# Kernel optimization log

Hardware: AMD Instinct MI355X
Metric: run time of the kernel (lower is better)

Reference implementation:

```python
import jax, jax.numpy as jnp
import numpy as np

B, S, D, DK, DV = 8, 2048, 256, 128, 128

def setup_inputs() -> dict:
    key = jax.random.key(0)
    ks = jax.random.split(key, 9)
    return {
        "x_q": jax.random.normal(ks[0], (B, S, D), jnp.float32),
        "x_k": jax.random.normal(ks[1], (B, S, D), jnp.float32),
        "x_v": jax.random.normal(ks[2], (B, S, D), jnp.float32),
        "Wq": jax.random.normal(ks[3], (D, DK), jnp.float32) * (1.0 / np.sqrt(D)),
        "bq": jax.random.normal(ks[4], (DK,), jnp.float32) * 0.02,
        "Wk": jax.random.normal(ks[5], (D, DK), jnp.float32) * (1.0 / np.sqrt(D)),
        "bk": jax.random.normal(ks[6], (DK,), jnp.float32) * 0.02,
        "Wv": jax.random.normal(ks[7], (D, DV), jnp.float32) * (1.0 / np.sqrt(D)),
        "bv": jax.random.normal(ks[8], (DV,), jnp.float32) * 0.02,
    }

def reference(x_q, x_k, x_v, Wq, bq, Wk, bk, Wv, bv):
    # Dense projections: [B,S,D] @ [D,dk] + bias
    q = jnp.einsum("bsd,dk->bsk", x_q, Wq) + bq
    k = jnp.einsum("bsd,dk->bsk", x_k, Wk) + bk
    v = jnp.einsum("bsd,dv->bsv", x_v, Wv) + bv
    scale = 1.0 / np.sqrt(Wq.shape[1]).astype(np.float32)  # 1/sqrt(d_k)
    scores = jnp.einsum("bqk,bsk->bqs", q, k) * scale       # [B,S,S]
    attn = jax.nn.softmax(scores, axis=-1)
    return jnp.einsum("bqs,bsv->bqv", attn, v)               # [B,S,d_v]
```

## Files before the change

kernel.cpp:

```cpp
#include <hip/hip_runtime.h>
#include <stdint.h>

typedef float    f32x4 __attribute__((ext_vector_type(4)));
typedef _Float16 f16x8 __attribute__((ext_vector_type(8)));
typedef _Float16 f16x4 __attribute__((ext_vector_type(4)));
typedef unsigned int u32x4 __attribute__((ext_vector_type(4)));

#define SPLIT 4
#define NTILES 8

__device__ __forceinline__ f32x4 mfma16(f16x8 a, f16x8 b, f32x4 c) {
    return __builtin_amdgcn_mfma_f32_16x16x32_f16(a, b, c, 0, 0, 0);
}
__device__ __forceinline__ f32x4 mfma16k16(f16x4 a, f16x4 b, f32x4 c) {
    return __builtin_amdgcn_mfma_f32_16x16x16f16(a, b, c, 0, 0, 0);
}
__device__ __forceinline__ void gll16(const _Float16* g, _Float16* l) {
    __builtin_amdgcn_global_load_lds(
        (const __attribute__((address_space(1))) void*)g,
        (__attribute__((address_space(3))) void*)l, 16, 0, 0);
}

__global__ __launch_bounds__(256) void prep_weights(
    const float* __restrict__ Wq, const float* __restrict__ Wk,
    const float* __restrict__ Wv, _Float16* __restrict__ wt) {
    __shared__ float Ls[64 * 65];
    const int bx = blockIdx.x;
    const int w  = bx >> 3, t = bx & 7;
    const int k0 = (t >> 1) * 64, n0 = (t & 1) * 64;
    const float* W = (w == 0) ? Wq : (w == 1) ? Wk : Wv;
    const int tid = threadIdx.x;
    #pragma unroll
    for (int i = 0; i < 16; i++) {
        int idx = i * 256 + tid;
        int r = idx >> 6, c = idx & 63;
        Ls[r * 65 + c] = W[(k0 + r) * 128 + n0 + c];
    }
    __syncthreads();
    #pragma unroll
    for (int i = 0; i < 16; i++) {
        int idx = i * 256 + tid;
        int r2 = idx >> 6, c2 = idx & 63;
        wt[w * 32768 + (n0 + r2) * 256 + k0 + c2] = (_Float16)Ls[c2 * 65 + r2];
    }
}

__global__ __launch_bounds__(256) void proj_kernel(
    const float* __restrict__ xq, const float* __restrict__ xk,
    const float* __restrict__ xv, const _Float16* __restrict__ wt,
    const float* __restrict__ bq, const float* __restrict__ bk,
    const float* __restrict__ bv,
    _Float16* __restrict__ qo, _Float16* __restrict__ ko,
    _Float16* __restrict__ vtmp)
{
    const int mode = blockIdx.y;
    const float*    X    = mode == 0 ? xq : mode == 1 ? xk : xv;
    const float*    bias = mode == 0 ? bq : mode == 1 ? bk : bv;
    const _Float16* W    = wt + mode * 32768;
    _Float16*       Y    = mode == 0 ? qo : mode == 1 ? ko : vtmp;

    const int tid  = threadIdx.x;
    const int wave = tid >> 6, lane = tid & 63;
    const int ln   = lane & 15, qd = lane >> 4;
    const int row0 = blockIdx.x * 64 + wave * 16;

    const float*    xrow = X + (size_t)(row0 + ln) * 256 + qd * 8;
    const _Float16* wb   = W + ln * 256 + qd * 8;

    f32x4 acc[8];
    #pragma unroll
    for (int i = 0; i < 8; i++) acc[i] = (f32x4){0.f, 0.f, 0.f, 0.f};

    #pragma unroll
    for (int kk = 0; kk < 8; kk++) {
        f32x4 a0 = *(const f32x4*)(xrow + kk * 32);
        f32x4 a1 = *(const f32x4*)(xrow + kk * 32 + 4);
        f16x8 af;
        af[0] = (_Float16)a0[0]; af[1] = (_Float16)a0[1];
        af[2] = (_Float16)a0[2]; af[3] = (_Float16)a0[3];
        af[4] = (_Float16)a1[0]; af[5] = (_Float16)a1[1];
        af[6] = (_Float16)a1[2]; af[7] = (_Float16)a1[3];
        #pragma unroll
        for (int nt = 0; nt < 8; nt++) {
            f16x8 bf = *(const f16x8*)(wb + nt * 4096 + kk * 32);
            acc[nt] = mfma16(af, bf, acc[nt]);
        }
    }

    const float SC = 0.08838834764831845f * 1.4426950408889634f;
    #pragma unroll
    for (int nt = 0; nt < 8; nt++) {
        int col = nt * 16 + ln;
        float bb = bias[col];
        #pragma unroll
        for (int r = 0; r < 4; r++) {
            int orow = row0 + qd * 4 + r;
            float val = acc[nt][r] + bb;
            if (mode == 0) val *= SC;
            Y[(size_t)orow * 128 + col] = (_Float16)val;
        }
    }
}

__global__ __launch_bounds__(256) void transpose_v(
    const _Float16* __restrict__ vtmp, _Float16* __restrict__ vt)
{
    __shared__ __align__(16) _Float16 Ls[64 * 72];
    const int b  = blockIdx.z;
    const int s0 = blockIdx.x * 64;
    const int d0 = blockIdx.y * 64;
    const int tid = threadIdx.x;
    #pragma unroll
    for (int i = 0; i < 2; i++) {
        int idx = i * 256 + tid;
        int r = idx >> 3, c = (idx & 7) * 8;
        *(f16x8*)&Ls[r * 72 + c] =
            *(const f16x8*)(vtmp + (size_t)(b * 2048 + s0 + r) * 128 + d0 + c);
    }
    __syncthreads();
    #pragma unroll
    for (int i = 0; i < 2; i++) {
        int idx = i * 256 + tid;
        int dr = idx >> 3, sc8 = (idx & 7) * 8;
        f16x8 o;
        #pragma unroll
        for (int j = 0; j < 8; j++) o[j] = Ls[(sc8 + j) * 72 + dr];
        *(f16x8*)(vt + (size_t)(b * 128 + d0 + dr) * 2048 + s0 + sc8) = o;
    }
}

__global__ __launch_bounds__(512, 4) void attn_kernel(
    const _Float16* __restrict__ qp, const _Float16* __restrict__ kp,
    const _Float16* __restrict__ vtp, _Float16* __restrict__ opart,
    float2* __restrict__ ml)
{
    const int bid = blockIdx.x;
    const int gx  = bid & 7;
    const int q0i = (bid >> 3) & 15;
    const int gg  = bid >> 7;
    const int g   = gg * 8 + gx;
    const int b   = g >> 2;
    const int z   = g & 3;
    const int q0  = q0i * 128;

    const int tid  = threadIdx.x;
    const int wave = tid >> 6, lane = tid & 63;
    const int ln   = lane & 15, qd = lane >> 4;

    __shared__ __align__(16) _Float16 smem[32768];

    const _Float16* qrow =
        qp + (size_t)(b * 2048 + q0 + wave * 16 + ln) * 128 + qd * 8;
    f16x8 qf[4];
    #pragma unroll
    for (int c = 0; c < 4; c++) qf[c] = *(const f16x8*)(qrow + c * 32);

    f32x4 o[8];
    #pragma unroll
    for (int i = 0; i < 8; i++) o[i] = (f32x4){0.f, 0.f, 0.f, 0.f};
    float m_run = -1e30f, l_run = 0.f;

    const _Float16* kbase = kp + (size_t)b * 2048 * 128;
    const _Float16* vbase = vtp + (size_t)b * 128 * 2048;
    const int kt0 = z * NTILES;

    auto stage = [&](int kt, int buf) {
        const _Float16* ks = kbase + (size_t)kt * 64 * 128;
        const _Float16* vs = vbase + kt * 64;
        _Float16* kdst0 = smem + buf * 8192;
        _Float16* vdst0 = smem + 16384 + buf * 8192;
        #pragma unroll
        for (int j = 0; j < 2; j++) {
            int p  = wave * 128 + j * 64 + lane;
            int r  = p >> 4, cp = p & 15;
            int cl = cp ^ (r & 15);
            gll16(ks + r * 128 + cl * 8, kdst0 + (wave * 128 + j * 64) * 8);
            int dv = p >> 3, cq = p & 7;
            int c2 = cq ^ (dv & 7);
            gll16(vs + (size_t)dv * 2048 + c2 * 8, vdst0 + (wave * 128 + j * 64) * 8);
        }
    };

    stage(kt0, 0);

    for (int it = 0; it < NTILES; it++) {
        __syncthreads();
        if (it + 1 < NTILES) stage(kt0 + it + 1, (it + 1) & 1);
        const _Float16* kb = smem + (it & 1) * 8192;
        const _Float16* vb = smem + 16384 + (it & 1) * 8192;

        f32x4 sc[4];
        #pragma unroll
        for (int st = 0; st < 4; st++) {
            sc[st] = (f32x4){0.f, 0.f, 0.f, 0.f};
            int base = (st * 16 + ln) * 128;
            #pragma unroll
            for (int c = 0; c < 4; c++) {
                f16x8 kf = *(const f16x8*)&kb[base + ((c * 4 + qd) ^ ln) * 8];
                sc[st] = mfma16(kf, qf[c], sc[st]);
            }
        }

        float t = sc[0][0];
        #pragma unroll
        for (int st = 0; st < 4; st++)
            #pragma unroll
            for (int r = 0; r < 4; r++) t = fmaxf(t, sc[st][r]);
        t = fmaxf(t, __shfl_xor(t, 16));
        t = fmaxf(t, __shfl_xor(t, 32));
        const float mnew  = fmaxf(m_run, t);
        const float alpha = exp2f(m_run - mnew);

        f16x4 ph[4];
        float ssum = 0.f;
        #pragma unroll
        for (int st = 0; st < 4; st++) {
            #pragma unroll
            for (int r = 0; r < 4; r++) {
                float p = exp2f(sc[st][r] - mnew);
                ssum += p;
                ph[st][r] = (_Float16)p;
            }
        }
        ssum += __shfl_xor(ssum, 16);
        ssum += __shfl_xor(ssum, 32);
        l_run = l_run * alpha + ssum;
        m_run = mnew;

        #pragma unroll
        for (int dt = 0; dt < 8; dt++)
            #pragma unroll
            for (int r = 0; r < 4; r++) o[dt][r] *= alpha;

        #pragma unroll
        for (int st = 0; st < 4; st++) {
            #pragma unroll
            for (int dt = 0; dt < 8; dt++) {
                f16x4 vf = *(const f16x4*)&vb[(dt * 16 + ln) * 64 +
                           ((st * 2 + (qd >> 1)) ^ (ln & 7)) * 8 + (qd & 1) * 4];
                o[dt] = mfma16k16(vf, ph[st], o[dt]);
            }
        }
    }

    __syncthreads();
    _Float16* pw = smem + wave * 2176;
    #pragma unroll
    for (int dt = 0; dt < 8; dt++) {
        f16x4 h;
        #pragma unroll
        for (int r = 0; r < 4; r++) h[r] = (_Float16)o[dt][r];
        *(f16x4*)&pw[ln * 136 + dt * 16 + qd * 4] = h;
    }
    const size_t prow = (size_t)(z * 8 + b) * 2048 + q0 + wave * 16;
    __builtin_amdgcn_s_waitcnt(0);
    #pragma unroll
    for (int i = 0; i < 4; i++) {
        int row = i * 4 + qd;
        f16x8 vrow = *(const f16x8*)&pw[row * 136 + ln * 8];
        *(f16x8*)(opart + (prow + row) * 128 + ln * 8) = vrow;
    }
    if (qd == 0) {
        float2 v; v.x = m_run; v.y = l_run;
        ml[prow + ln] = v;
    }
}

__global__ __launch_bounds__(256) void merge_kernel(
    const _Float16* __restrict__ opart, const float2* __restrict__ ml,
    float* __restrict__ out)
{
    const int t = threadIdx.x;
    const int r = t >> 4, cg = t & 15;
    const size_t row = (size_t)blockIdx.x * 16 + r;

    float M = -1e30f;
    #pragma unroll
    for (int zi = 0; zi < SPLIT; zi++)
        M = fmaxf(M, ml[(size_t)zi * 16384 + row].x);
    float L = 0.f;
    float acc[8] = {0.f, 0.f, 0.f, 0.f, 0.f, 0.f, 0.f, 0.f};
    #pragma unroll
    for (int zi = 0; zi < SPLIT; zi++) {
        float2 p = ml[(size_t)zi * 16384 + row];
        float w = exp2f(p.x - M);
        L += w * p.y;
        f16x8 v = *(const f16x8*)&opart[((size_t)zi * 16384 + row) * 128 + cg * 8];
        #pragma unroll
        for (int j = 0; j < 8; j++) acc[j] += w * (float)v[j];
    }
    const float inv = 1.0f / L;
    float* op = out + row * 128 + cg * 8;
    f32x4 lo = (f32x4){acc[0] * inv, acc[1] * inv, acc[2] * inv, acc[3] * inv};
    f32x4 hi = (f32x4){acc[4] * inv, acc[5] * inv, acc[6] * inv, acc[7] * inv};
    *(f32x4*)op = lo;
    *(f32x4*)(op + 4) = hi;
}

extern "C" void kernel_launch(void* const* d_in, const int* in_sizes, int n_in,
                              void* d_out, int out_size, void* d_ws, size_t ws_size,
                              hipStream_t stream) {
    const float* xq = (const float*)d_in[0];
    const float* xk = (const float*)d_in[1];
    const float* xv = (const float*)d_in[2];
    const float* Wq = (const float*)d_in[3];
    const float* bq = (const float*)d_in[4];
    const float* Wk = (const float*)d_in[5];
    const float* bk = (const float*)d_in[6];
    const float* Wv = (const float*)d_in[7];
    const float* bv = (const float*)d_in[8];
    float* out = (float*)d_out;

    char* ws = (char*)d_ws;
    _Float16* wt    = (_Float16*)ws;
    _Float16* qo    = (_Float16*)(ws + 196608);
    _Float16* ko    = (_Float16*)(ws + 196608 + 4194304);
    _Float16* vt    = (_Float16*)(ws + 196608 + 2 * 4194304);
    float2*   ml    = (float2*)  (ws + 196608 + 3 * 4194304);
    _Float16* opart = (_Float16*)(ws + 196608 + 3 * 4194304 + 1048576);
    _Float16* vtmp  = opart;

    hipLaunchKernelGGL(prep_weights, dim3(24), dim3(256), 0, stream,
                       Wq, Wk, Wv, wt);
    hipLaunchKernelGGL(proj_kernel, dim3(256, 3), dim3(256), 0, stream,
                       xq, xk, xv, wt, bq, bk, bv, qo, ko, vtmp);
    hipLaunchKernelGGL(transpose_v, dim3(32, 2, 8), dim3(256), 0, stream,
                       vtmp, vt);
    hipLaunchKernelGGL(attn_kernel, dim3(16 * 8 * SPLIT), dim3(512), 0, stream,
                       qo, ko, vt, opart, ml);
    hipLaunchKernelGGL(merge_kernel, dim3(1024), dim3(256), 0, stream,
                       opart, ml, out);
}
```

Measured before the change: 164.0 us.

## Switch attention to 32x32x16 MFMA tiles with 8-way KV split

Rewrites the attention kernel around 32x32x16 f16 MFMAs, so each wave owns 32 query rows and processes 32-key tiles, up from 16x16 MFMAs on 16 rows. P fragments are exchanged between half-waves with a shuffle so they can feed the PV MFMA. The block shrinks to 256 threads with a smaller LDS footprint, and the KV split goes from 4 to 8, doubling the grid. The aim is fewer MFMA and LDS instructions per FLOP and better occupancy. In exchange, the partial-output traffic and merge work double, and the V tile layout in LDS is no longer XOR-swizzled, which may cause bank conflicts.

```diff
diff --git a/kernel.cpp b/kernel.cpp
--- a/kernel.cpp
+++ b/kernel.cpp
@@ -1,19 +1,20 @@
 #include <hip/hip_runtime.h>
 #include <stdint.h>
 
-typedef float    f32x4 __attribute__((ext_vector_type(4)));
-typedef _Float16 f16x8 __attribute__((ext_vector_type(8)));
-typedef _Float16 f16x4 __attribute__((ext_vector_type(4)));
+typedef float    f32x4  __attribute__((ext_vector_type(4)));
+typedef float    f32x16 __attribute__((ext_vector_type(16)));
+typedef _Float16 f16x8  __attribute__((ext_vector_type(8)));
+typedef _Float16 f16x4  __attribute__((ext_vector_type(4)));
 typedef unsigned int u32x4 __attribute__((ext_vector_type(4)));
 
-#define SPLIT 4
+#define SPLIT 8
 #define NTILES 8
 
 __device__ __forceinline__ f32x4 mfma16(f16x8 a, f16x8 b, f32x4 c) {
     return __builtin_amdgcn_mfma_f32_16x16x32_f16(a, b, c, 0, 0, 0);
 }
-__device__ __forceinline__ f32x4 mfma16k16(f16x4 a, f16x4 b, f32x4 c) {
-    return __builtin_amdgcn_mfma_f32_16x16x16f16(a, b, c, 0, 0, 0);
+__device__ __forceinline__ f32x16 mfma32(f16x8 a, f16x8 b, f32x16 c) {
+    return __builtin_amdgcn_mfma_f32_32x32x16_f16(a, b, c, 0, 0, 0);
 }
 __device__ __forceinline__ void gll16(const _Float16* g, _Float16* l) {
     __builtin_amdgcn_global_load_lds(
@@ -129,7 +130,7 @@
     }
 }
 
-__global__ __launch_bounds__(512, 4) void attn_kernel(
+__global__ __launch_bounds__(256, 3) void attn_kernel(
     const _Float16* __restrict__ qp, const _Float16* __restrict__ kp,
     const _Float16* __restrict__ vtp, _Float16* __restrict__ opart,
     float2* __restrict__ ml)
@@ -139,25 +140,25 @@
     const int q0i = (bid >> 3) & 15;
     const int gg  = bid >> 7;
     const int g   = gg * 8 + gx;
-    const int b   = g >> 2;
-    const int z   = g & 3;
+    const int b   = g >> 3;
+    const int z   = g & 7;
     const int q0  = q0i * 128;
 
     const int tid  = threadIdx.x;
     const int wave = tid >> 6, lane = tid & 63;
-    const int ln   = lane & 15, qd = lane >> 4;
-
-    __shared__ __align__(16) _Float16 smem[32768];
-
-    const _Float16* qrow =
-        qp + (size_t)(b * 2048 + q0 + wave * 16 + ln) * 128 + qd * 8;
-    f16x8 qf[4];
-    #pragma unroll
-    for (int c = 0; c < 4; c++) qf[c] = *(const f16x8*)(qrow + c * 32);
-
-    f32x4 o[8];
-    #pragma unroll
-    for (int i = 0; i < 8; i++) o[i] = (f32x4){0.f, 0.f, 0.f, 0.f};
+    const int ln   = lane & 31, h = lane >> 5;
+
+    __shared__ __align__(16) _Float16 smem[16896];
+
+    const _Float16* qbase =
+        qp + (size_t)(b * 2048 + q0 + wave * 32 + ln) * 128 + h * 8;
+    f16x8 qf[8];
+    #pragma unroll
+    for (int kb = 0; kb < 8; kb++) qf[kb] = *(const f16x8*)(qbase + kb * 16);
+
+    f32x16 o[4];
+    #pragma unroll
+    for (int i = 0; i < 4; i++) o[i] = (f32x16){};
     float m_run = -1e30f, l_run = 0.f;
 
     const _Float16* kbase = kp + (size_t)b * 2048 * 128;
@@ -165,19 +166,18 @@
     const int kt0 = z * NTILES;
 
     auto stage = [&](int kt, int buf) {
-        const _Float16* ks = kbase + (size_t)kt * 64 * 128;
-        const _Float16* vs = vbase + kt * 64;
-        _Float16* kdst0 = smem + buf * 8192;
-        _Float16* vdst0 = smem + 16384 + buf * 8192;
+        const _Float16* ks = kbase + (size_t)kt * 4096;
+        const _Float16* vs = vbase + kt * 32;
+        _Float16* kdst = smem + buf * 4096;
+        _Float16* vdst = smem + 8192 + buf * 4096;
         #pragma unroll
         for (int j = 0; j < 2; j++) {
             int p  = wave * 128 + j * 64 + lane;
-            int r  = p >> 4, cp = p & 15;
-            int cl = cp ^ (r & 15);
-            gll16(ks + r * 128 + cl * 8, kdst0 + (wave * 128 + j * 64) * 8);
-            int dv = p >> 3, cq = p & 7;
-            int c2 = cq ^ (dv & 7);
-            gll16(vs + (size_t)dv * 2048 + c2 * 8, vdst0 + (wave * 128 + j * 64) * 8);
+            int r  = p >> 4, c = p & 15;
+            int cs = c ^ (r & 15);
+            gll16(ks + r * 128 + cs * 8, kdst + (wave * 128 + j * 64) * 8);
+            int rv = p >> 2, cv = p & 3;
+            gll16(vs + (size_t)rv * 2048 + cv * 8, vdst + (wave * 128 + j * 64) * 8);
         }
     };
 
@@ -186,81 +186,85 @@
     for (int it = 0; it < NTILES; it++) {
         __syncthreads();
         if (it + 1 < NTILES) stage(kt0 + it + 1, (it + 1) & 1);
-        const _Float16* kb = smem + (it & 1) * 8192;
-        const _Float16* vb = smem + 16384 + (it & 1) * 8192;
-
-        f32x4 sc[4];
-        #pragma unroll
-        for (int st = 0; st < 4; st++) {
-            sc[st] = (f32x4){0.f, 0.f, 0.f, 0.f};
-            int base = (st * 16 + ln) * 128;
-            #pragma unroll
-            for (int c = 0; c < 4; c++) {
-                f16x8 kf = *(const f16x8*)&kb[base + ((c * 4 + qd) ^ ln) * 8];
-                sc[st] = mfma16(kf, qf[c], sc[st]);
-            }
-        }
-
-        float t = sc[0][0];
-        #pragma unroll
-        for (int st = 0; st < 4; st++)
-            #pragma unroll
-            for (int r = 0; r < 4; r++) t = fmaxf(t, sc[st][r]);
-        t = fmaxf(t, __shfl_xor(t, 16));
+        const _Float16* kb_ = smem + (it & 1) * 4096;
+        const _Float16* vb_ = smem + 8192 + (it & 1) * 4096;
+
+        f32x16 sc = (f32x16){};
+        #pragma unroll
+        for (int kb = 0; kb < 8; kb++) {
+            int phys = (kb * 2 + h) ^ (ln & 15);
+            f16x8 kf = *(const f16x8*)&kb_[ln * 128 + phys * 8];
+            sc = mfma32(kf, qf[kb], sc);
+        }
+
+        float t = sc[0];
+        #pragma unroll
+        for (int i = 1; i < 16; i++) t = fmaxf(t, sc[i]);
         t = fmaxf(t, __shfl_xor(t, 32));
         const float mnew  = fmaxf(m_run, t);
         const float alpha = exp2f(m_run - mnew);
 
-        f16x4 ph[4];
+        f16x4 phg[4];
         float ssum = 0.f;
         #pragma unroll
-        for (int st = 0; st < 4; st++) {
+        for (int gi = 0; gi < 4; gi++) {
             #pragma unroll
-            for (int r = 0; r < 4; r++) {
-                float p = exp2f(sc[st][r] - mnew);
+            for (int e = 0; e < 4; e++) {
+                float p = exp2f(sc[gi * 4 + e] - mnew);
                 ssum += p;
-                ph[st][r] = (_Float16)p;
+                phg[gi][e] = (_Float16)p;
             }
         }
-        ssum += __shfl_xor(ssum, 16);
         ssum += __shfl_xor(ssum, 32);
         l_run = l_run * alpha + ssum;
         m_run = mnew;
 
         #pragma unroll
-        for (int dt = 0; dt < 8; dt++)
+        for (int dvb = 0; dvb < 4; dvb++) o[dvb] *= alpha;
+
+        #pragma unroll
+        for (int kb2 = 0; kb2 < 2; kb2++) {
+            f16x4 own0 = phg[2 * kb2], own1 = phg[2 * kb2 + 1];
+            f16x4 send = h ? own0 : own1;
+            unsigned long long sv = __builtin_bit_cast(unsigned long long, send);
+            unsigned long long rv = __shfl_xor(sv, 32);
+            f16x4 recv = __builtin_bit_cast(f16x4, rv);
+            f16x4 lo = h ? recv : own0;
+            f16x4 hi = h ? own1 : recv;
+            f16x8 bf = __builtin_shufflevector(lo, hi, 0, 1, 2, 3, 4, 5, 6, 7);
             #pragma unroll
-            for (int r = 0; r < 4; r++) o[dt][r] *= alpha;
-
-        #pragma unroll
-        for (int st = 0; st < 4; st++) {
+            for (int dvb = 0; dvb < 4; dvb++) {
+                f16x8 vf = *(const f16x8*)&vb_[(dvb * 32 + ln) * 32 +
+                                               (kb2 * 2 + h) * 8];
+                o[dvb] = mfma32(vf, bf, o[dvb]);
+            }
+        }
+    }
+
+    __syncthreads();
+    _Float16* pw = smem + wave * 4224;
+    #pragma unroll
+    for (int dvb = 0; dvb < 4; dvb++) {
+        #pragma unroll
+        for (int gi = 0; gi < 4; gi++) {
+            f16x4 w4;
             #pragma unroll
-            for (int dt = 0; dt < 8; dt++) {
-                f16x4 vf = *(const f16x4*)&vb[(dt * 16 + ln) * 64 +
-                           ((st * 2 + (qd >> 1)) ^ (ln & 7)) * 8 + (qd & 1) * 4];
-                o[dt] = mfma16k16(vf, ph[st], o[dt]);
-            }
-        }
-    }
-
-    __syncthreads();
-    _Float16* pw = smem + wave * 2176;
-    #pragma unroll
-    for (int dt = 0; dt < 8; dt++) {
-        f16x4 h;
-        #pragma unroll
-        for (int r = 0; r < 4; r++) h[r] = (_Float16)o[dt][r];
-        *(f16x4*)&pw[ln * 136 + dt * 16 + qd * 4] = h;
-    }
-    const size_t prow = (size_t)(z * 8 + b) * 2048 + q0 + wave * 16;
+            for (int e = 0; e < 4; e++) w4[e] = (_Float16)o[dvb][gi * 4 + e];
+            *(f16x4*)&pw[ln * 132 + dvb * 32 + gi * 8 + h * 4] = w4;
+        }
+    }
+    const size_t prow = (size_t)(z * 8 + b) * 2048 + q0 + wave * 32;
     __builtin_amdgcn_s_waitcnt(0);
     #pragma unroll
-    for (int i = 0; i < 4; i++) {
-        int row = i * 4 + qd;
-        f16x8 vrow = *(const f16x8*)&pw[row * 136 + ln * 8];
-        *(f16x8*)(opart + (prow + row) * 128 + ln * 8) = vrow;
-    }
-    if (qd == 0) {
+    for (int p = 0; p < 2; p++) {
+        int q = p * 16 + (lane >> 2), part = lane & 3;
+        #pragma unroll
+        for (int i2 = 0; i2 < 4; i2++) {
+            f16x8 v8 = *(const f16x8*)&pw[q * 132 + part * 8 + i2 * 32];
+            *(f16x8*)(opart + (prow + q) * 128 + part * 8 + i2 * 32) = v8;
+        }
+    }
+    if (lane < 32) {
         float2 v; v.x = m_run; v.y = l_run;
         ml[prow + ln] = v;
     }
@@ -326,7 +330,7 @@
                        xq, xk, xv, wt, bq, bk, bv, qo, ko, vtmp);
     hipLaunchKernelGGL(transpose_v, dim3(32, 2, 8), dim3(256), 0, stream,
                        vtmp, vt);
-    hipLaunchKernelGGL(attn_kernel, dim3(16 * 8 * SPLIT), dim3(512), 0, stream,
+    hipLaunchKernelGGL(attn_kernel, dim3(16 * 8 * SPLIT), dim3(256), 0, stream,
                        qo, ko, vt, opart, ml);
     hipLaunchKernelGGL(merge_kernel, dim3(1024), dim3(256), 0, stream,
                        opart, ml, out);
```

After: 167.4 us. +2.1%, slower.
